# Kernel optimization log

Measured on AMD Instinct MI355X. Metric: run time of the kernel, lower is better.

Reference implementation:

```python
import jax, jax.numpy as jnp
import numpy as np

N_NODES = 131072
HIDDEN = 256
N_CLUSTERS = 64
NUM_GRAPHS = 64
MAX_NODES = 4096  # static pad length (>= max nodes per graph w.h.p.)


def setup_inputs() -> dict:
    key = jax.random.key(0)
    ks = jax.random.split(key, 12)
    d = HIDDEN
    xav = (6.0 / (2 * d)) ** 0.5  # xavier_uniform bound for square Linear / Q param
    x = jax.random.normal(ks[0], (N_NODES, d), dtype=jnp.float32)
    batch = jnp.sort(jax.random.randint(ks[1], (N_NODES,), 0, NUM_GRAPHS)).astype(jnp.int64)
    def lin(kw, kb):
        W = jax.random.uniform(kw, (d, d), dtype=jnp.float32, minval=-xav, maxval=xav)
        b = jax.random.uniform(kb, (d,), dtype=jnp.float32, minval=-d ** -0.5, maxval=d ** -0.5)
        return W, b
    Qp = jax.random.uniform(ks[2], (1, N_CLUSTERS, d), dtype=jnp.float32, minval=-xav, maxval=xav)
    WQ_w, WQ_b = lin(ks[3], ks[4])
    WK_w, WK_b = lin(ks[5], ks[6])
    WV_w, WV_b = lin(ks[7], ks[8])
    WO_w, WO_b = lin(ks[9], ks[10])
    return {"x": x, "batch": batch, "Qp": Qp,
            "WQ_w": WQ_w, "WQ_b": WQ_b, "WK_w": WK_w, "WK_b": WK_b,
            "WV_w": WV_w, "WV_b": WV_b, "WO_w": WO_w, "WO_b": WO_b}


def _dense_pos(batch):
    # position of each node within its graph (batch is sorted)
    ones = jnp.ones_like(batch, dtype=jnp.int32)
    counts = jax.ops.segment_sum(ones, batch, num_segments=NUM_GRAPHS)
    starts = jnp.cumsum(counts) - counts
    pos = jnp.arange(batch.shape[0], dtype=jnp.int32) - starts[batch]
    return pos


def reference(x, batch, Qp, WQ_w, WQ_b, WK_w, WK_b, WV_w, WV_b, WO_w, WO_b):
    d = x.shape[-1]
    pos = _dense_pos(batch)
    K = x @ WK_w.T + WK_b
    V = x @ WV_w.T + WV_b
    # to_dense_batch: scatter into [B, MAX_NODES, d] (out-of-range dropped)
    Kd = jnp.zeros((NUM_GRAPHS, MAX_NODES, d), x.dtype).at[batch, pos].set(K, mode='drop')
    Vd = jnp.zeros((NUM_GRAPHS, MAX_NODES, d), x.dtype).at[batch, pos].set(V, mode='drop')
    mask = jnp.zeros((NUM_GRAPHS, MAX_NODES), bool).at[batch, pos].set(True, mode='drop')
    attn_mask = (~mask).astype(x.dtype)[:, None, :] * (-1e9)  # [B,1,L]
    Q = jnp.broadcast_to(Qp, (NUM_GRAPHS, N_CLUSTERS, d)) @ WQ_w.T + WQ_b  # [B,C,d]
    A = jnp.einsum('bcd,bld->bcl', Q, Kd) / (d ** 0.5) + attn_mask
    A = jax.nn.softmax(A, axis=-2)  # inverted softmax: over cluster (query) axis
    out = Q + jnp.einsum('bcl,bld->bcd', A, Vd)
    out = jax.nn.relu(out @ WO_w.T + WO_b)  # residual=False branch
    return out, jnp.argmax(A, axis=-2), mask
```

## Files before the change

### kernel.cpp

```cpp
#include <hip/hip_runtime.h>

#define N_NODES 131072
#define MAXL 4096
#define NP 8

typedef __attribute__((ext_vector_type(8))) short bf16x8;
typedef __attribute__((ext_vector_type(4))) float f32x4;

#define OFF_QW     0u
#define OFF_QO     16384u
#define OFF_WF     32768u
#define OFF_QB     98304u
#define OFF_BVO    98368u
#define OFF_STARTS 98624u
#define OFF_ASUM   98752u
#define OFF_Q      102848u
#define OFF_WQT    119232u
#define OFF_WOT    184768u
#define OFF_GP     250304u

__device__ __forceinline__ unsigned short f2bf(float f) {
  union { float f; unsigned int u; } v; v.f = f;
  unsigned int u = v.u + 0x7FFFu + ((v.u >> 16) & 1u);
  return (unsigned short)(u >> 16);
}

__device__ __forceinline__ float dppx1(float v) {
  return __int_as_float(__builtin_amdgcn_update_dpp(0, __float_as_int(v), 0xB1, 0xF, 0xF, true));
}
__device__ __forceinline__ float dppx2(float v) {
  return __int_as_float(__builtin_amdgcn_update_dpp(0, __float_as_int(v), 0x4E, 0xF, 0xF, true));
}
__device__ __forceinline__ float swzx4(float v) {
  return __int_as_float(__builtin_amdgcn_ds_swizzle(__float_as_int(v), 0x101F));
}
__device__ __forceinline__ float kq_sum(float v) {
  v += dppx1(v); v += dppx2(v); v += swzx4(v); return v;
}
__device__ __forceinline__ float mrg1(float u, float v, bool sel) {
  float snd = sel ? u : v, kp = sel ? v : u; return kp + dppx1(snd);
}
__device__ __forceinline__ float mrg2(float u, float v, bool sel) {
  float snd = sel ? u : v, kp = sel ? v : u; return kp + dppx2(snd);
}
__device__ __forceinline__ float mrg4(float u, float v, bool sel) {
  float snd = sel ? u : v, kp = sel ? v : u; return kp + swzx4(snd);
}


__global__ __launch_bounds__(256) void k_tr(const float* __restrict__ WQ_w,
    const float* __restrict__ WO_w, float* __restrict__ WQT, float* __restrict__ WOT)
{
  __shared__ float tile[32][33];
  const float* src = blockIdx.z ? WO_w : WQ_w;
  float* dst = blockIdx.z ? WOT : WQT;
  const int bx = blockIdx.x * 32, by = blockIdx.y * 32;
  const int tx = threadIdx.x & 31, ty = threadIdx.x >> 5;
  #pragma unroll
  for (int i = 0; i < 4; ++i)
    tile[ty + 8 * i][tx] = src[(size_t)(by + ty + 8 * i) * 256 + bx + tx];
  __syncthreads();
  #pragma unroll
  for (int i = 0; i < 4; ++i)
    dst[(size_t)(bx + ty + 8 * i) * 256 + by + tx] = tile[tx][ty + 8 * i];
}

__global__ __launch_bounds__(1024) void k_q(const float* __restrict__ Qp,
    const float* __restrict__ WQT, const float* __restrict__ WQ_b,
    float* __restrict__ Q)
{
  __shared__ float red[4][256];
  const int c = blockIdx.x, t = threadIdx.x;
  const int d = t & 255, kk = t >> 8;
  float acc = 0.f;
  #pragma unroll 4
  for (int k = kk * 64; k < kk * 64 + 64; ++k)
    acc += Qp[c * 256 + k] * WQT[k * 256 + d];
  red[kk][d] = acc;
  __syncthreads();
  if (kk == 0)
    Q[c * 256 + d] = red[0][d] + red[1][d] + red[2][d] + red[3][d] + WQ_b[d];
}

__global__ __launch_bounds__(1024) void k_fold(const float* __restrict__ Q,
    const float* __restrict__ WK_w, const float* __restrict__ WK_b,
    const float* __restrict__ WOT,
    float* __restrict__ QW, float* __restrict__ QO, float* __restrict__ qb)
{
  __shared__ float Qrow[256];
  __shared__ double redw[4][256];
  __shared__ float redo[4][256];
  const int c = blockIdx.x, t = threadIdx.x;
  const int d = t & 255, kk = t >> 8;
  if (t < 256) Qrow[t] = Q[c * 256 + t];
  __syncthreads();
  double aqw = 0.0;
  float aqo = 0.f;
  #pragma unroll 4
  for (int j = kk * 64; j < kk * 64 + 64; ++j) {
    float qcj = Qrow[j];
    aqw += (double)qcj * (double)WK_w[j * 256 + d];
    aqo += qcj * WOT[j * 256 + d];
  }
  redw[kk][d] = aqw;
  redo[kk][d] = aqo;
  __syncthreads();
  if (kk == 0) {
    QW[c * 256 + d] = (float)((redw[0][d] + redw[1][d] + redw[2][d] + redw[3][d]) * 0.0625);
    QO[c * 256 + d] = redo[0][d] + redo[1][d] + redo[2][d] + redo[3][d];
  }
  __syncthreads();
  if (t < 256) redw[0][t] = (double)Qrow[t] * (double)WK_b[t];
  __syncthreads();
  for (int sft = 128; sft >= 1; sft >>= 1) {
    if (t < sft) redw[0][t] += redw[0][t + sft];
    __syncthreads();
  }
  if (t == 0) qb[c] = (float)(redw[0][0] * 0.0625);
}

__global__ __launch_bounds__(1024) void k_wf(const float* __restrict__ WO_w,
    const float* __restrict__ WV_w, const float* __restrict__ WV_b,
    float* __restrict__ Wf, float* __restrict__ bvo)
{
  __shared__ float red[4][256];
  __shared__ float redb[4];
  const int i = blockIdx.x, t = threadIdx.x;
  const int d = t & 255, kk = t >> 8;
  float acc = 0.f;
  #pragma unroll 4
  for (int j = kk * 64; j < kk * 64 + 64; ++j)
    acc += WO_w[i * 256 + j] * WV_w[j * 256 + d];
  red[kk][d] = acc;
  if (d == 0) {
    float s = 0.f;
    for (int j = kk * 64; j < kk * 64 + 64; ++j) s += WV_b[j] * WO_w[i * 256 + j];
    redb[kk] = s;
  }
  __syncthreads();
  if (kk == 0) {
    Wf[i * 256 + d] = red[0][d] + red[1][d] + red[2][d] + red[3][d];
    if (d == 0) bvo[i] = redb[0] + redb[1] + redb[2] + redb[3];
  }
}

__global__ void k_starts(const int* __restrict__ batch, int* __restrict__ starts)
{
  int t = threadIdx.x;
  if (t > 64) return;
  if (t == 0) { starts[0] = 0; return; }
  if (t == 64) { starts[64] = N_NODES; return; }
  int lo = 0, hi = N_NODES;
  while (lo < hi) {
    int mid = (lo + hi) >> 1;
    if (batch[mid] < t) lo = mid + 1; else hi = mid;
  }
  starts[t] = lo;
}


__global__ __launch_bounds__(512, 4) void k_fused(
    const float* __restrict__ x, const int* __restrict__ starts,
    const float* __restrict__ qw, const float* __restrict__ qbv,
    float* __restrict__ Gp, float* __restrict__ asum,
    float* __restrict__ out_arg, float* __restrict__ out_msk)
{
  __shared__ float xs[32][256];
  __shared__ float ss[32][68];
  __shared__ float stats_m[32], stats_i[32];
  __shared__ __align__(16) unsigned short As[64][40];
  __shared__ __align__(16) unsigned short XsT[256][40];

  const int t = threadIdx.x;
  const int p = blockIdx.x, b = blockIdx.y;
  const int s0 = starts[b], s1 = starts[b + 1];
  const int w = t >> 6, lane = t & 63;
  const int wg = w & 3, wh = w >> 2;
  const int cp = lane >> 3, kq = lane & 7;
  const int c0 = wg * 16 + cp, c1 = c0 + 8;

  const float qb0 = qbv[c0], qb1 = qbv[c1];
  const float* qg0 = qw + (size_t)c0 * 256 + kq * 16;
  const float* qg1 = qw + (size_t)c1 * 256 + kq * 16;

  f32x4 gacc[8];
  #pragma unroll
  for (int i = 0; i < 8; ++i) gacc[i] = (f32x4){0.f, 0.f, 0.f, 0.f};
  float asv0 = 0.f, asv1 = 0.f;

  const bool sel1 = (kq & 1), sel2 = (kq & 2), sel4 = (kq & 4);
  const int stcol = (lane * 4) ^ (4 * ((lane >> 3) & 7));
  const int dX = t & 255, hX = t >> 8;
  const int dsz = dX ^ (4 * ((dX >> 5) & 7));

  #pragma unroll 1
  for (int base = s0 + p * 32; base < s1; base += NP * 32) {
    #pragma unroll
    for (int i = 0; i < 4; ++i) {
      int r = w * 4 + i;
      int gr = base + r; if (gr >= s1) gr = s1 - 1;
      float4 v = *(const float4*)&x[(size_t)gr * 256 + lane * 4];
      *(float4*)&xs[r][stcol] = v;
    }
    __syncthreads();
    #pragma unroll
    for (int g = 0; g < 4; ++g) {
      const int r0 = hX * 16 + g * 4;
      ushort4 pk;
      pk.x = f2bf(xs[r0 + 0][dsz]);
      pk.y = f2bf(xs[r0 + 1][dsz]);
      pk.z = f2bf(xs[r0 + 2][dsz]);
      pk.w = f2bf(xs[r0 + 3][dsz]);
      *(ushort4*)&XsT[dX][r0] = pk;
    }
    #pragma unroll 1
    for (int nb = 0; nb < 4; ++nb) {
      float a0[4], a1[4];
      #pragma unroll
      for (int n = 0; n < 4; ++n) { a0[n] = 0.f; a1[n] = 0.f; }
      const float* xb = &xs[wh * 16 + nb * 4][0];
      #pragma unroll 1
      for (int h2 = 0; h2 < 2; ++h2) {
        {
          float4 qa0 = *(const float4*)&qg0[h2 * 128 + 0];
          float4 qa1 = *(const float4*)&qg0[h2 * 128 + 4];
          float4 qc0 = *(const float4*)&qg1[h2 * 128 + 0];
          float4 qc1 = *(const float4*)&qg1[h2 * 128 + 4];
          #pragma unroll
          for (int k4 = 0; k4 < 2; ++k4) {
            const int colb = h2 * 128 + kq * 16 + k4 * 4;
            const int col = colb ^ (4 * ((colb >> 5) & 7));
            const float4 qa = k4 ? qa1 : qa0;
            const float4 qc = k4 ? qc1 : qc0;
            #pragma unroll
            for (int n = 0; n < 4; ++n) {
              float4 xv = *(const float4*)&xb[n * 256 + col];
              a0[n] = fmaf(qa.w, xv.w, fmaf(qa.z, xv.z, fmaf(qa.y, xv.y, fmaf(qa.x, xv.x, a0[n]))));
              a1[n] = fmaf(qc.w, xv.w, fmaf(qc.z, xv.z, fmaf(qc.y, xv.y, fmaf(qc.x, xv.x, a1[n]))));
            }
          }
        }
        {
          float4 qa2 = *(const float4*)&qg0[h2 * 128 + 8];
          float4 qa3 = *(const float4*)&qg0[h2 * 128 + 12];
          float4 qc2 = *(const float4*)&qg1[h2 * 128 + 8];
          float4 qc3 = *(const float4*)&qg1[h2 * 128 + 12];
          #pragma unroll
          for (int k4 = 2; k4 < 4; ++k4) {
            const int colb = h2 * 128 + kq * 16 + k4 * 4;
            const int col = colb ^ (4 * ((colb >> 5) & 7));
            const float4 qa = (k4 == 2) ? qa2 : qa3;
            const float4 qc = (k4 == 2) ? qc2 : qc3;
            #pragma unroll
            for (int n = 0; n < 4; ++n) {
              float4 xv = *(const float4*)&xb[n * 256 + col];
              a0[n] = fmaf(qa.w, xv.w, fmaf(qa.z, xv.z, fmaf(qa.y, xv.y, fmaf(qa.x, xv.x, a0[n]))));
              a1[n] = fmaf(qc.w, xv.w, fmaf(qc.z, xv.z, fmaf(qc.y, xv.y, fmaf(qc.x, xv.x, a1[n]))));
            }
          }
        }
      }
      {
        float r00 = mrg1(a0[0], a0[1], sel1);
        float r01 = mrg1(a0[2], a0[3], sel1);
        float r10 = mrg1(a1[0], a1[1], sel1);
        float r11 = mrg1(a1[2], a1[3], sel1);
        float t0  = mrg2(r00, r01, sel2);
        float t1  = mrg2(r10, r11, sel2);
        float val = mrg4(t0, t1, sel4);
        const int nn = wh * 16 + nb * 4 + (kq & 3);
        ss[nn][sel4 ? c1 : c0] = val + (sel4 ? qb1 : qb0);
      }
    }
    __syncthreads();
    if (t < 256) {
      const int nn = t >> 3, oct = t & 7;
      float v8[8];
      #pragma unroll
      for (int u = 0; u < 8; ++u) v8[u] = ss[nn][oct * 8 + u];
      float m = v8[0]; int am = oct * 8;
      #pragma unroll
      for (int u = 1; u < 8; ++u)
        if (v8[u] > m) { m = v8[u]; am = oct * 8 + u; }
      #pragma unroll
      for (int d = 1; d < 8; d <<= 1) {
        float mo = __shfl_xor(m, d);
        int ao = __shfl_xor(am, d);
        if (mo > m || (mo == m && ao < am)) { m = mo; am = ao; }
      }
      float s = 0.f;
      #pragma unroll
      for (int u = 0; u < 8; ++u) s += __expf(v8[u] - m);
      #pragma unroll
      for (int d = 1; d < 8; d <<= 1) s += __shfl_xor(s, d);
      if (oct == 0) {
        stats_m[nn] = m;
        stats_i[nn] = 1.f / s;
        int n = base + nn;
        if (n < s1) {
          int pos = n - s0;
          out_arg[(size_t)b * MAXL + pos] = (float)am;
          out_msk[(size_t)b * MAXL + pos] = 1.0f;
        }
      }
    }
    __syncthreads();
    {
      unsigned short pb0[2], pb1[2];
      #pragma unroll
      for (int i = 0; i < 2; ++i) {
        int nn = 4 * kq + 2 * wh + i;
        bool valid = (base + nn) < s1;
        float m = stats_m[nn], inv = stats_i[nn];
        float av0 = valid ? __expf(ss[nn][c0] - m) * inv : 0.f;
        float av1 = valid ? __expf(ss[nn][c1] - m) * inv : 0.f;
        asv0 += av0; asv1 += av1;
        pb0[i] = f2bf(av0);
        pb1[i] = f2bf(av1);
      }
      *(ushort2*)&As[c0][4 * kq + 2 * wh] = *(const ushort2*)pb0;
      *(ushort2*)&As[c1][4 * kq + 2 * wh] = *(const ushort2*)pb1;
    }
    __syncthreads();
    {
      const int q = lane >> 4, mm = lane & 15;
      bf16x8 afrag = *(const bf16x8*)&As[16 * wg + mm][q * 8];
      #pragma unroll
      for (int dt2 = 0; dt2 < 8; ++dt2) {
        const int dt = wh * 8 + dt2;
        bf16x8 bfrag = *(const bf16x8*)&XsT[16 * dt + mm][q * 8];
        gacc[dt2] = __builtin_amdgcn_mfma_f32_16x16x32_bf16(afrag, bfrag, gacc[dt2], 0, 0, 0);
      }
    }
    __syncthreads();
  }

  {
    float* g = Gp + ((size_t)p * 64 + b) * 16384;
    const int q = lane >> 4, mm = lane & 15;
    #pragma unroll
    for (int dt2 = 0; dt2 < 8; ++dt2) {
      const int dt = wh * 8 + dt2;
      #pragma unroll
      for (int r = 0; r < 4; ++r)
        g[(size_t)(16 * wg + q * 4 + r) * 256 + 16 * dt + mm] = gacc[dt2][r];
    }
  }
  asv0 = kq_sum(asv0);
  asv1 = kq_sum(asv1);
  if (kq == 0) {
    atomicAdd(&asum[b * 64 + c0], asv0);
    atomicAdd(&asum[b * 64 + c1], asv1);
  }
}


__global__ __launch_bounds__(256) void k_final(const float* __restrict__ Gp,
    int npart, const float* __restrict__ Wf, const float* __restrict__ qo,
    const float* __restrict__ asum, const float* __restrict__ bvo,
    const float* __restrict__ WO_b, float* __restrict__ out)
{
  __shared__ float gs[64 * 68];
  __shared__ float wfs[64 * 68];
  const int t = threadIdx.x;
  const int b = blockIdx.x >> 2;
  const int is = (blockIdx.x & 3) * 64;
  const int tx = t & 15, ty = t >> 4;
  const int sr = t >> 4, sq = t & 15;

  float acc[4][4];
  #pragma unroll
  for (int j = 0; j < 4; ++j)
    #pragma unroll
    for (int u = 0; u < 4; ++u) acc[j][u] = 0.f;

  for (int kc = 0; kc < 4; ++kc) {
    const int k0 = kc * 64;
    #pragma unroll
    for (int u = 0; u < 4; ++u) {
      int row = sr + 16 * u;
      float4 g = make_float4(0.f, 0.f, 0.f, 0.f);
      for (int p = 0; p < npart; ++p) {
        float4 gv = *(const float4*)&Gp[((size_t)p * 64 + b) * 16384
                                        + row * 256 + k0 + sq * 4];
        g.x += gv.x; g.y += gv.y; g.z += gv.z; g.w += gv.w;
      }
      *(float4*)&gs[row * 68 + sq * 4] = g;
      *(float4*)&wfs[row * 68 + sq * 4] =
          *(const float4*)&Wf[(size_t)(is + row) * 256 + k0 + sq * 4];
    }
    __syncthreads();
    #pragma unroll
    for (int k4 = 0; k4 < 16; ++k4) {
      float4 gr[4], wr[4];
      #pragma unroll
      for (int j = 0; j < 4; ++j) gr[j] = *(const float4*)&gs[(ty + 16 * j) * 68 + k4 * 4];
      #pragma unroll
      for (int u = 0; u < 4; ++u) wr[u] = *(const float4*)&wfs[(tx + 16 * u) * 68 + k4 * 4];
      #pragma unroll
      for (int j = 0; j < 4; ++j)
        #pragma unroll
        for (int u = 0; u < 4; ++u)
          acc[j][u] += gr[j].x * wr[u].x + gr[j].y * wr[u].y
                     + gr[j].z * wr[u].z + gr[j].w * wr[u].w;
    }
    __syncthreads();
  }

  #pragma unroll
  for (int j = 0; j < 4; ++j)
    #pragma unroll
    for (int u = 0; u < 4; ++u) {
      int cc = ty + 16 * j, i = is + tx + 16 * u;
      float v = acc[j][u] + qo[cc * 256 + i] + asum[b * 64 + cc] * bvo[i] + WO_b[i];
      out[(size_t)b * 16384 + cc * 256 + i] = fmaxf(v, 0.f);
    }
}


extern "C" void kernel_launch(void* const* d_in, const int* in_sizes, int n_in,
                              void* d_out, int out_size, void* d_ws, size_t ws_size,
                              hipStream_t stream) {
  const float* x    = (const float*)d_in[0];
  const int*   batch= (const int*)d_in[1];
  const float* Qp   = (const float*)d_in[2];
  const float* WQ_w = (const float*)d_in[3];
  const float* WQ_b = (const float*)d_in[4];
  const float* WK_w = (const float*)d_in[5];
  const float* WK_b = (const float*)d_in[6];
  const float* WV_w = (const float*)d_in[7];
  const float* WV_b = (const float*)d_in[8];
  const float* WO_w = (const float*)d_in[9];
  const float* WO_b = (const float*)d_in[10];

  float* ws   = (float*)d_ws;
  float* QW   = ws + OFF_QW;
  float* QO   = ws + OFF_QO;
  float* Wf   = ws + OFF_WF;
  float* qb   = ws + OFF_QB;
  float* bvo  = ws + OFF_BVO;
  int*   starts = (int*)(ws + OFF_STARTS);
  float* asum = ws + OFF_ASUM;
  float* Q    = ws + OFF_Q;
  float* WQT  = ws + OFF_WQT;
  float* WOT  = ws + OFF_WOT;
  float* Gp   = ws + OFF_GP;

  float* out     = (float*)d_out;
  float* out_arg = out + 64 * 64 * 256;
  float* out_msk = out_arg + 64 * MAXL;

  hipMemsetAsync(asum, 0, 64 * 64 * sizeof(float), stream);
  hipMemsetAsync(out_arg, 0, (size_t)2 * 64 * MAXL * sizeof(float), stream);

  k_tr<<<dim3(8, 8, 2), 256, 0, stream>>>(WQ_w, WO_w, WQT, WOT);
  k_wf<<<256, 1024, 0, stream>>>(WO_w, WV_w, WV_b, Wf, bvo);
  k_starts<<<1, 128, 0, stream>>>(batch, starts);
  k_q<<<64, 1024, 0, stream>>>(Qp, WQT, WQ_b, Q);
  k_fold<<<64, 1024, 0, stream>>>(Q, WK_w, WK_b, WOT, QW, QO, qb);

  k_fused<<<dim3(NP, 64), 512, 0, stream>>>(x, starts, QW, qb, Gp, asum,
                                            out_arg, out_msk);
  k_final<<<64 * 4, 256, 0, stream>>>(Gp, NP, Wf, QO, asum, bvo, WO_b, out);
}
```

Baseline: 435.4 us.

## Merge prep kernels into one launch and register-block query weights in fused scoring

After: 382.9 us. 1.14x faster.

```diff
diff --git a/kernel.cpp b/kernel.cpp
--- a/kernel.cpp
+++ b/kernel.cpp
@@ -65,101 +65,93 @@
     dst[(size_t)(bx + ty + 8 * i) * 256 + by + tx] = tile[tx][ty + 8 * i];
 }
 
-__global__ __launch_bounds__(1024) void k_q(const float* __restrict__ Qp,
-    const float* __restrict__ WQT, const float* __restrict__ WQ_b,
-    float* __restrict__ Q)
-{
-  __shared__ float red[4][256];
-  const int c = blockIdx.x, t = threadIdx.x;
-  const int d = t & 255, kk = t >> 8;
-  float acc = 0.f;
-  #pragma unroll 4
-  for (int k = kk * 64; k < kk * 64 + 64; ++k)
-    acc += Qp[c * 256 + k] * WQT[k * 256 + d];
-  red[kk][d] = acc;
-  __syncthreads();
-  if (kk == 0)
-    Q[c * 256 + d] = red[0][d] + red[1][d] + red[2][d] + red[3][d] + WQ_b[d];
-}
-
-__global__ __launch_bounds__(1024) void k_fold(const float* __restrict__ Q,
+__global__ __launch_bounds__(1024) void k_prep(
+    const float* __restrict__ Qp, const float* __restrict__ WQT,
+    const float* __restrict__ WQ_b,
     const float* __restrict__ WK_w, const float* __restrict__ WK_b,
     const float* __restrict__ WOT,
-    float* __restrict__ QW, float* __restrict__ QO, float* __restrict__ qb)
+    const float* __restrict__ WO_w, const float* __restrict__ WV_w,
+    const float* __restrict__ WV_b,
+    const int* __restrict__ batch,
+    float* __restrict__ QW, float* __restrict__ QO, float* __restrict__ qb,
+    float* __restrict__ Wf, float* __restrict__ bvo, int* __restrict__ starts)
 {
-  __shared__ float Qrow[256];
-  __shared__ double redw[4][256];
-  __shared__ float redo[4][256];
-  const int c = blockIdx.x, t = threadIdx.x;
+  const int bid = blockIdx.x, t = threadIdx.x;
   const int d = t & 255, kk = t >> 8;
-  if (t < 256) Qrow[t] = Q[c * 256 + t];
-  __syncthreads();
-  double aqw = 0.0;
-  float aqo = 0.f;
-  #pragma unroll 4
-  for (int j = kk * 64; j < kk * 64 + 64; ++j) {
-    float qcj = Qrow[j];
-    aqw += (double)qcj * (double)WK_w[j * 256 + d];
-    aqo += qcj * WOT[j * 256 + d];
-  }
-  redw[kk][d] = aqw;
-  redo[kk][d] = aqo;
-  __syncthreads();
-  if (kk == 0) {
-    QW[c * 256 + d] = (float)((redw[0][d] + redw[1][d] + redw[2][d] + redw[3][d]) * 0.0625);
-    QO[c * 256 + d] = redo[0][d] + redo[1][d] + redo[2][d] + redo[3][d];
-  }
-  __syncthreads();
-  if (t < 256) redw[0][t] = (double)Qrow[t] * (double)WK_b[t];
-  __syncthreads();
-  for (int sft = 128; sft >= 1; sft >>= 1) {
-    if (t < sft) redw[0][t] += redw[0][t + sft];
-    __syncthreads();
-  }
-  if (t == 0) qb[c] = (float)(redw[0][0] * 0.0625);
-}
-
-__global__ __launch_bounds__(1024) void k_wf(const float* __restrict__ WO_w,
-    const float* __restrict__ WV_w, const float* __restrict__ WV_b,
-    float* __restrict__ Wf, float* __restrict__ bvo)
-{
-  __shared__ float red[4][256];
-  __shared__ float redb[4];
-  const int i = blockIdx.x, t = threadIdx.x;
-  const int d = t & 255, kk = t >> 8;
-  float acc = 0.f;
-  #pragma unroll 4
-  for (int j = kk * 64; j < kk * 64 + 64; ++j)
-    acc += WO_w[i * 256 + j] * WV_w[j * 256 + d];
-  red[kk][d] = acc;
-  if (d == 0) {
-    float s = 0.f;
-    for (int j = kk * 64; j < kk * 64 + 64; ++j) s += WV_b[j] * WO_w[i * 256 + j];
-    redb[kk] = s;
-  }
-  __syncthreads();
-  if (kk == 0) {
-    Wf[i * 256 + d] = red[0][d] + red[1][d] + red[2][d] + red[3][d];
-    if (d == 0) bvo[i] = redb[0] + redb[1] + redb[2] + redb[3];
-  }
-}
-
-__global__ void k_starts(const int* __restrict__ batch, int* __restrict__ starts)
-{
-  int t = threadIdx.x;
-  if (t > 64) return;
-  if (t == 0) { starts[0] = 0; return; }
-  if (t == 64) { starts[64] = N_NODES; return; }
-  int lo = 0, hi = N_NODES;
-  while (lo < hi) {
-    int mid = (lo + hi) >> 1;
-    if (batch[mid] < t) lo = mid + 1; else hi = mid;
-  }
-  starts[t] = lo;
-}
-
-
-__global__ __launch_bounds__(512, 4) void k_fused(
+
+  if (bid < 64) {
+    __shared__ float Qrow[256];
+    __shared__ double redw[4][256];
+    __shared__ float redo[4][256];
+    const int c = bid;
+    {
+      float acc = 0.f;
+      #pragma unroll 4
+      for (int k = kk * 64; k < kk * 64 + 64; ++k)
+        acc += Qp[c * 256 + k] * WQT[k * 256 + d];
+      redo[kk][d] = acc;
+    }
+    __syncthreads();
+    if (kk == 0)
+      Qrow[d] = redo[0][d] + redo[1][d] + redo[2][d] + redo[3][d] + WQ_b[d];
+    __syncthreads();
+    double aqw = 0.0;
+    float aqo = 0.f;
+    #pragma unroll 4
+    for (int j = kk * 64; j < kk * 64 + 64; ++j) {
+      float qcj = Qrow[j];
+      aqw += (double)qcj * (double)WK_w[j * 256 + d];
+      aqo += qcj * WOT[j * 256 + d];
+    }
+    redw[kk][d] = aqw;
+    redo[kk][d] = aqo;
+    __syncthreads();
+    if (kk == 0) {
+      QW[c * 256 + d] = (float)((redw[0][d] + redw[1][d] + redw[2][d] + redw[3][d]) * 0.0625);
+      QO[c * 256 + d] = redo[0][d] + redo[1][d] + redo[2][d] + redo[3][d];
+    }
+    __syncthreads();
+    if (t < 256) redw[0][t] = (double)Qrow[t] * (double)WK_b[t];
+    __syncthreads();
+    for (int sft = 128; sft >= 1; sft >>= 1) {
+      if (t < sft) redw[0][t] += redw[0][t + sft];
+      __syncthreads();
+    }
+    if (t == 0) qb[c] = (float)(redw[0][0] * 0.0625);
+  } else if (bid < 320) {
+    __shared__ float red[4][256];
+    __shared__ float redb[4];
+    const int i = bid - 64;
+    float acc = 0.f;
+    #pragma unroll 4
+    for (int j = kk * 64; j < kk * 64 + 64; ++j)
+      acc += WO_w[i * 256 + j] * WV_w[j * 256 + d];
+    red[kk][d] = acc;
+    if (d == 0) {
+      float s = 0.f;
+      for (int j = kk * 64; j < kk * 64 + 64; ++j) s += WV_b[j] * WO_w[i * 256 + j];
+      redb[kk] = s;
+    }
+    __syncthreads();
+    if (kk == 0) {
+      Wf[i * 256 + d] = red[0][d] + red[1][d] + red[2][d] + red[3][d];
+      if (d == 0) bvo[i] = redb[0] + redb[1] + redb[2] + redb[3];
+    }
+  } else {
+    if (t > 64) return;
+    if (t == 0) { starts[0] = 0; return; }
+    if (t == 64) { starts[64] = N_NODES; return; }
+    int lo = 0, hi = N_NODES;
+    while (lo < hi) {
+      int mid = (lo + hi) >> 1;
+      if (batch[mid] < t) lo = mid + 1; else hi = mid;
+    }
+    starts[t] = lo;
+  }
+}
+
+
+__global__ __launch_bounds__(512, 2) void k_fused(
     const float* __restrict__ x, const int* __restrict__ starts,
     const float* __restrict__ qw, const float* __restrict__ qbv,
     float* __restrict__ Gp, float* __restrict__ asum,
@@ -178,17 +170,31 @@
   const int wg = w & 3, wh = w >> 2;
   const int cp = lane >> 3, kq = lane & 7;
   const int c0 = wg * 16 + cp, c1 = c0 + 8;
-
   const float qb0 = qbv[c0], qb1 = qbv[c1];
-  const float* qg0 = qw + (size_t)c0 * 256 + kq * 16;
-  const float* qg1 = qw + (size_t)c1 * 256 + kq * 16;
+
+  const int wgS = w & 1, whS = w >> 1;
+  const bool sel1 = (kq & 1), sel2 = (kq & 2), sel4 = (kq & 4);
+  const int cBase = wgS * 32 + cp;
+  const int czA = cBase + (sel4 ? 8 : 0);
+  const int czB = czA + 16;
+  const float qbzA = qbv[czA], qbzB = qbv[czB];
+
+  float4 qr[4][2][4];
+  #pragma unroll
+  for (int j = 0; j < 4; ++j) {
+    const float* qgj = qw + (size_t)(cBase + 8 * j) * 256 + kq * 16;
+    #pragma unroll
+    for (int h2 = 0; h2 < 2; ++h2)
+      #pragma unroll
+      for (int k4 = 0; k4 < 4; ++k4)
+        qr[j][h2][k4] = *(const float4*)&qgj[h2 * 128 + k4 * 4];
+  }
 
   f32x4 gacc[8];
   #pragma unroll
   for (int i = 0; i < 8; ++i) gacc[i] = (f32x4){0.f, 0.f, 0.f, 0.f};
   float asv0 = 0.f, asv1 = 0.f;
 
-  const bool sel1 = (kq & 1), sel2 = (kq & 2), sel4 = (kq & 4);
   const int stcol = (lane * 4) ^ (4 * ((lane >> 3) & 7));
   const int dX = t & 255, hX = t >> 8;
   const int dsz = dX ^ (4 * ((dX >> 5) & 7));
@@ -214,62 +220,51 @@
       *(ushort4*)&XsT[dX][r0] = pk;
     }
     #pragma unroll 1
-    for (int nb = 0; nb < 4; ++nb) {
-      float a0[4], a1[4];
-      #pragma unroll
-      for (int n = 0; n < 4; ++n) { a0[n] = 0.f; a1[n] = 0.f; }
-      const float* xb = &xs[wh * 16 + nb * 4][0];
-      #pragma unroll 1
+    for (int nb = 0; nb < 2; ++nb) {
+      float acc[4][4];
+      #pragma unroll
+      for (int j = 0; j < 4; ++j)
+        #pragma unroll
+        for (int n = 0; n < 4; ++n) acc[j][n] = 0.f;
+      const float* xb = &xs[whS * 8 + nb * 4][0];
+      #pragma unroll
       for (int h2 = 0; h2 < 2; ++h2) {
-        {
-          float4 qa0 = *(const float4*)&qg0[h2 * 128 + 0];
-          float4 qa1 = *(const float4*)&qg0[h2 * 128 + 4];
-          float4 qc0 = *(const float4*)&qg1[h2 * 128 + 0];
-          float4 qc1 = *(const float4*)&qg1[h2 * 128 + 4];
+        #pragma unroll
+        for (int k4 = 0; k4 < 4; ++k4) {
+          const int colb = h2 * 128 + kq * 16 + k4 * 4;
+          const int col = colb ^ (4 * ((colb >> 5) & 7));
+          const float4 q0 = qr[0][h2][k4];
+          const float4 q1 = qr[1][h2][k4];
+          const float4 q2 = qr[2][h2][k4];
+          const float4 q3 = qr[3][h2][k4];
           #pragma unroll
-          for (int k4 = 0; k4 < 2; ++k4) {
-            const int colb = h2 * 128 + kq * 16 + k4 * 4;
-            const int col = colb ^ (4 * ((colb >> 5) & 7));
-            const float4 qa = k4 ? qa1 : qa0;
-            const float4 qc = k4 ? qc1 : qc0;
-            #pragma unroll
-            for (int n = 0; n < 4; ++n) {
-              float4 xv = *(const float4*)&xb[n * 256 + col];
-              a0[n] = fmaf(qa.w, xv.w, fmaf(qa.z, xv.z, fmaf(qa.y, xv.y, fmaf(qa.x, xv.x, a0[n]))));
-              a1[n] = fmaf(qc.w, xv.w, fmaf(qc.z, xv.z, fmaf(qc.y, xv.y, fmaf(qc.x, xv.x, a1[n]))));
-            }
+          for (int n = 0; n < 4; ++n) {
+            float4 xv = *(const float4*)&xb[n * 256 + col];
+            acc[0][n] = fmaf(q0.w, xv.w, fmaf(q0.z, xv.z, fmaf(q0.y, xv.y, fmaf(q0.x, xv.x, acc[0][n]))));
+            acc[1][n] = fmaf(q1.w, xv.w, fmaf(q1.z, xv.z, fmaf(q1.y, xv.y, fmaf(q1.x, xv.x, acc[1][n]))));
+            acc[2][n] = fmaf(q2.w, xv.w, fmaf(q2.z, xv.z, fmaf(q2.y, xv.y, fmaf(q2.x, xv.x, acc[2][n]))));
+            acc[3][n] = fmaf(q3.w, xv.w, fmaf(q3.z, xv.z, fmaf(q3.y, xv.y, fmaf(q3.x, xv.x, acc[3][n]))));
           }
         }
-        {
-          float4 qa2 = *(const float4*)&qg0[h2 * 128 + 8];
-          float4 qa3 = *(const float4*)&qg0[h2 * 128 + 12];
-          float4 qc2 = *(const float4*)&qg1[h2 * 128 + 8];
-          float4 qc3 = *(const float4*)&qg1[h2 * 128 + 12];
-          #pragma unroll
-          for (int k4 = 2; k4 < 4; ++k4) {
-            const int colb = h2 * 128 + kq * 16 + k4 * 4;
-            const int col = colb ^ (4 * ((colb >> 5) & 7));
-            const float4 qa = (k4 == 2) ? qa2 : qa3;
-            const float4 qc = (k4 == 2) ? qc2 : qc3;
-            #pragma unroll
-            for (int n = 0; n < 4; ++n) {
-              float4 xv = *(const float4*)&xb[n * 256 + col];
-              a0[n] = fmaf(qa.w, xv.w, fmaf(qa.z, xv.z, fmaf(qa.y, xv.y, fmaf(qa.x, xv.x, a0[n]))));
-              a1[n] = fmaf(qc.w, xv.w, fmaf(qc.z, xv.z, fmaf(qc.y, xv.y, fmaf(qc.x, xv.x, a1[n]))));
-            }
-          }
-        }
       }
       {
-        float r00 = mrg1(a0[0], a0[1], sel1);
-        float r01 = mrg1(a0[2], a0[3], sel1);
-        float r10 = mrg1(a1[0], a1[1], sel1);
-        float r11 = mrg1(a1[2], a1[3], sel1);
-        float t0  = mrg2(r00, r01, sel2);
-        float t1  = mrg2(r10, r11, sel2);
-        float val = mrg4(t0, t1, sel4);
-        const int nn = wh * 16 + nb * 4 + (kq & 3);
-        ss[nn][sel4 ? c1 : c0] = val + (sel4 ? qb1 : qb0);
+        float r0 = mrg1(acc[0][0], acc[0][1], sel1);
+        float r1 = mrg1(acc[0][2], acc[0][3], sel1);
+        float r2 = mrg1(acc[1][0], acc[1][1], sel1);
+        float r3 = mrg1(acc[1][2], acc[1][3], sel1);
+        float r4 = mrg1(acc[2][0], acc[2][1], sel1);
+        float r5 = mrg1(acc[2][2], acc[2][3], sel1);
+        float r6 = mrg1(acc[3][0], acc[3][1], sel1);
+        float r7 = mrg1(acc[3][2], acc[3][3], sel1);
+        float w0 = mrg2(r0, r1, sel2);
+        float w1 = mrg2(r2, r3, sel2);
+        float w2 = mrg2(r4, r5, sel2);
+        float w3 = mrg2(r6, r7, sel2);
+        float z0 = mrg4(w0, w1, sel4);
+        float z1 = mrg4(w2, w3, sel4);
+        const int nn = whS * 8 + nb * 4 + (kq & 3);
+        ss[nn][czA] = z0 + qbzA;
+        ss[nn][czB] = z1 + qbzB;
       }
     }
     __syncthreads();
@@ -441,7 +436,6 @@
   float* bvo  = ws + OFF_BVO;
   int*   starts = (int*)(ws + OFF_STARTS);
   float* asum = ws + OFF_ASUM;
-  float* Q    = ws + OFF_Q;
   float* WQT  = ws + OFF_WQT;
   float* WOT  = ws + OFF_WOT;
   float* Gp   = ws + OFF_GP;
@@ -454,10 +448,9 @@
   hipMemsetAsync(out_arg, 0, (size_t)2 * 64 * MAXL * sizeof(float), stream);
 
   k_tr<<<dim3(8, 8, 2), 256, 0, stream>>>(WQ_w, WO_w, WQT, WOT);
-  k_wf<<<256, 1024, 0, stream>>>(WO_w, WV_w, WV_b, Wf, bvo);
-  k_starts<<<1, 128, 0, stream>>>(batch, starts);
-  k_q<<<64, 1024, 0, stream>>>(Qp, WQT, WQ_b, Q);
-  k_fold<<<64, 1024, 0, stream>>>(Q, WK_w, WK_b, WOT, QW, QO, qb);
+  k_prep<<<321, 1024, 0, stream>>>(Qp, WQT, WQ_b, WK_w, WK_b, WOT,
+                                   WO_w, WV_w, WV_b, batch,
+                                   QW, QO, qb, Wf, bvo, starts);
 
   k_fused<<<dim3(NP, 64), 512, 0, stream>>>(x, starts, QW, qb, Gp, asum,
                                             out_arg, out_msk);
```
